# Optimization experiments

Hardware: AMD Instinct MI355X
Metric: run time of the kernel (lower is better)

The kernel has to match this reference:

```python
import jax, jax.numpy as jnp
import numpy as np

B, G, L, S = 4096, 16000, 64, 20000  # batch spots, genes, labels, total spots
LOG_2PI = float(np.log(2.0 * np.pi))


def _log_nb_positive_altparam(x, r, o):
    # NB with total_count r > 0 and logits o (stereoscope parametrization)
    return (jax.lax.lgamma(x + r) - jax.lax.lgamma(r) - jax.lax.lgamma(x + 1.0)
            + x * jax.nn.log_sigmoid(o) + r * jax.nn.log_sigmoid(-o))


def setup_inputs() -> dict:
    key = jax.random.key(0)
    ks = jax.random.split(key, 8)
    x = jax.random.randint(ks[0], (B, G), 0, 100, dtype=jnp.int32)
    y = jax.random.randint(ks[1], (B, 1), 0, L, dtype=jnp.int32)
    ind_x = jax.random.randint(ks[2], (B, 1), 0, S, dtype=jnp.int32)
    W = jax.random.normal(ks[3], (G, L), dtype=jnp.float32)          # fixed dictionary
    px_o = 0.5 * jax.random.normal(ks[4], (G,), dtype=jnp.float32)   # fixed log-odds
    eta = jax.random.normal(ks[5], (G,), dtype=jnp.float32)
    V = jax.random.normal(ks[6], (L + 1, S), dtype=jnp.float32)
    beta = 0.1 * jax.random.normal(ks[7], (G,), dtype=jnp.float32)
    return {"x": x, "y": y, "ind_x": ind_x, "W": W, "px_o": px_o,
            "eta": eta, "V": V, "beta": beta}


def reference(x, y, ind_x, W, px_o, eta, V, beta):
    x_f = x.astype(jnp.float32)                      # [B, G]
    beta_sp = jax.nn.softplus(beta)                  # [G]
    w_sp = jax.nn.softplus(W)                        # [G, L]
    eps_sp = jax.nn.softplus(eta)                    # [G]
    # r_hat = [beta*W | eps]  -> [G, L+1]
    r_hat = jnp.concatenate([beta_sp[:, None] * w_sp, eps_sp[:, None]], axis=1)
    # column-gather from V (embedding lookup over spots), then softplus
    v_ind = jax.nn.softplus(V[:, ind_x[:, 0]])       # [L+1, B]
    # thin matmul, inner dim L+1; px_rate: [B, G]
    px_rate = jnp.einsum("gl,lb->bg", r_hat, v_ind)
    # NB reconstruction loss per spot
    reconst_loss = -jnp.sum(_log_nb_positive_altparam(x_f, px_rate, px_o[None, :]), axis=-1)  # [B]
    # -sum log N(eta; 0, 1)
    neg_log_likelihood_prior = jnp.sum(0.5 * LOG_2PI + 0.5 * eta * eta)
    return (reconst_loss, jnp.float32(0.0), neg_log_likelihood_prior)
```

## Files before the change

### kernel.cpp

```cpp
#include <hip/hip_runtime.h>
#include <hip/hip_bf16.h>
#include <math.h>

#define Gn 16000
#define Bn 4096
#define Ln 64
#define Sn 20000

typedef __attribute__((ext_vector_type(8))) short bf16x8;
typedef __attribute__((ext_vector_type(4))) float f32x4;


__device__ __forceinline__ float softplus_precise(float z) {
    return fmaxf(z, 0.0f) + log1pf(__expf(-fabsf(z)));
}

__device__ __forceinline__ float lgamma_pos8(float z) {
    float p = z * (z + 1.f) * (z + 2.f) * (z + 3.f)
                * (z + 4.f) * (z + 5.f) * (z + 6.f) * (z + 7.f);
    float w = z + 8.f;
    return (w - 0.5f) * __logf(w) - w + 0.9189385332046727f
           + __fdividef(1.0f, 12.0f * w) - __logf(p);
}

__device__ __forceinline__ unsigned short f2bf(float f) {
    union { float f; unsigned int u; } v; v.f = f;
    unsigned int r = v.u + 0x7fff + ((v.u >> 16) & 1);
    return (unsigned short)(r >> 16);
}


__global__ void prep_genes(const float* __restrict__ W,
                           const float* __restrict__ px_o,
                           const float* __restrict__ eta,
                           const float* __restrict__ beta,
                           unsigned short* __restrict__ rhB,
                           float* __restrict__ lsp,
                           float* __restrict__ lsn,
                           float* __restrict__ eps) {
    int idx = blockIdx.x * 256 + threadIdx.x;
    int g = idx >> 6;
    float bsp = softplus_precise(beta[g]);
    rhB[idx] = f2bf(bsp * softplus_precise(W[idx]));
    if (idx < Gn) {
        eps[idx] = softplus_precise(eta[idx]);
        float o = px_o[idx];
        lsp[idx] = -softplus_precise(-o);
        lsn[idx] = -softplus_precise(o);
    }
}

__global__ void prep_spots(const float* __restrict__ V,
                           const int* __restrict__ ind_x,
                           unsigned short* __restrict__ vBg,
                           float* __restrict__ v64) {
    int idx = blockIdx.x * 256 + threadIdx.x;
    int b = idx >> 6, l = idx & 63;
    int s = ind_x[b];
    vBg[idx] = f2bf(softplus_precise(V[l * Sn + s]));
    if (idx < Bn) {
        int s2 = ind_x[idx];
        v64[idx] = softplus_precise(V[Ln * Sn + s2]);
    }
}

__global__ void prior_kernel(const float* __restrict__ eta, float* __restrict__ out) {
    int tid = threadIdx.x;
    float s = 0.f;
    for (int g = tid; g < Gn; g += 256) {
        float e = eta[g];
        s += 0.9189385332046727f + 0.5f * e * e;
    }
    #pragma unroll
    for (int off = 32; off; off >>= 1) s += __shfl_xor(s, off, 64);
    __shared__ float red[4];
    if ((tid & 63) == 0) red[tid >> 6] = s;
    __syncthreads();
    if (tid == 0) {
        out[Bn]     = 0.0f;
        out[Bn + 1] = red[0] + red[1] + red[2] + red[3];
    }
}


__global__ __launch_bounds__(256) void main_kernel(
    const int*            __restrict__ x,
    const unsigned short* __restrict__ rhB,
    const unsigned short* __restrict__ vBg,
    const float*          __restrict__ v64,
    const float*          __restrict__ lspg,
    const float*          __restrict__ lsng,
    const float*          __restrict__ epsg,
    float*                __restrict__ out) {
    __shared__ __align__(16) unsigned short sA[64][72];
    __shared__ __align__(16) unsigned short sB[64][72];
    __shared__ float sv64[64];
    __shared__ float sLsp[64], sLsn[64], sEps[64];
    __shared__ float lfact[100];

    const int tid = threadIdx.x;
    const int g0 = blockIdx.x * 64;
    const int b0 = blockIdx.y * 64;

    {
        int row = tid >> 3;
        int c   = (tid & 7) * 8;
        *(uint4*)&sA[row][c]      = *(const uint4*)&vBg[(b0 + row) * 64 + c];
        *(uint4*)&sA[row + 32][c] = *(const uint4*)&vBg[(b0 + row + 32) * 64 + c];
        *(uint4*)&sB[row][c]      = *(const uint4*)&rhB[(g0 + row) * 64 + c];
        *(uint4*)&sB[row + 32][c] = *(const uint4*)&rhB[(g0 + row + 32) * 64 + c];
    }
    if (tid < 64) {
        sv64[tid] = v64[b0 + tid];
        sLsp[tid] = lspg[g0 + tid];
        sLsn[tid] = lsng[g0 + tid];
        sEps[tid] = epsg[g0 + tid];
    }
    if (tid < 100) lfact[tid] = lgamma_pos8((float)tid + 1.0f);

    const int wave = tid >> 6, lane = tid & 63;
    const int quad = lane >> 4, ln = lane & 15;
    const int mrow  = wave * 16 + ln;
    const int brow0 = b0 + wave * 16 + quad * 4;

    int xv[4][4];
    #pragma unroll
    for (int nb = 0; nb < 4; nb++) {
        int g = g0 + nb * 16 + ln;
        #pragma unroll
        for (int r = 0; r < 4; r++)
            xv[nb][r] = x[(brow0 + r) * Gn + g];
    }

    f32x4 acc[4];
    #pragma unroll
    for (int nb = 0; nb < 4; nb++) acc[nb] = (f32x4){0.f, 0.f, 0.f, 0.f};

    __syncthreads();

    #pragma unroll
    for (int kb = 0; kb < 2; kb++) {
        bf16x8 af = *(const bf16x8*)&sA[mrow][kb * 32 + quad * 8];
        #pragma unroll
        for (int nb = 0; nb < 4; nb++) {
            bf16x8 bf = *(const bf16x8*)&sB[nb * 16 + ln][kb * 32 + quad * 8];
            acc[nb] = __builtin_amdgcn_mfma_f32_16x16x32_bf16(af, bf, acc[nb], 0, 0, 0);
        }
    }

    float vvr[4];
    #pragma unroll
    for (int r = 0; r < 4; r++) vvr[r] = sv64[wave * 16 + quad * 4 + r];

    float rowpart[4] = {0.f, 0.f, 0.f, 0.f};
    #pragma unroll
    for (int nb = 0; nb < 4; nb++) {
        const float lspv = sLsp[nb * 16 + ln];
        const float lsnv = sLsn[nb * 16 + ln];
        const float ev   = sEps[nb * 16 + ln];
        #pragma unroll
        for (int r = 0; r < 4; r++) {
            const float rr = fmaf(ev, vvr[r], acc[nb][r]);
            const int   xi = xv[nb][r];
            const float xf = (float)xi;
            const float s  = rr + xf;
            const float wr = rr + 4.f, wx = s + 4.f;
            const float Pr = rr * (rr + 1.f) * ((rr + 2.f) * (rr + 3.f));
            const float Px = s  * (s  + 1.f) * ((s  + 2.f) * (s  + 3.f));
            const float lnQ = __logf(__fdividef(Px, Pr));
            float D = fmaf(wx - 0.5f, __logf(wx), -fmaf(wr - 0.5f, __logf(wr), xf))
                      - lnQ - 0.0833333333f * __fdividef(xf, wx * wr);
            float term = D - lfact[xi] + fmaf(xf, lspv, rr * lsnv);
            rowpart[r] += term;
        }
    }

    #pragma unroll
    for (int r = 0; r < 4; r++) {
        float v = rowpart[r];
        v += __shfl_xor(v, 1, 64);
        v += __shfl_xor(v, 2, 64);
        v += __shfl_xor(v, 4, 64);
        v += __shfl_xor(v, 8, 64);
        if (ln == 0) atomicAdd(&out[brow0 + r], -v);
    }
}


extern "C" void kernel_launch(void* const* d_in, const int* in_sizes, int n_in,
                              void* d_out, int out_size, void* d_ws, size_t ws_size,
                              hipStream_t stream) {
    const int*   x     = (const int*)d_in[0];
    const int*   ind_x = (const int*)d_in[2];
    const float* W     = (const float*)d_in[3];
    const float* px_o  = (const float*)d_in[4];
    const float* eta   = (const float*)d_in[5];
    const float* V     = (const float*)d_in[6];
    const float* beta  = (const float*)d_in[7];
    float* out = (float*)d_out;

    char* wsb = (char*)d_ws;
    unsigned short* rhB = (unsigned short*)(wsb);
    unsigned short* vBg = (unsigned short*)(wsb + 2048000);
    float*          v64 = (float*)(wsb + 2572288);
    float*          lsp = (float*)(wsb + 2588672);
    float*          lsn = (float*)(wsb + 2652672);
    float*          eps = (float*)(wsb + 2716672);

    hipMemsetAsync(d_out, 0, Bn * sizeof(float), stream);

    prep_genes<<<(Gn * 64) / 256, 256, 0, stream>>>(W, px_o, eta, beta, rhB, lsp, lsn, eps);
    prep_spots<<<(Bn * 64) / 256, 256, 0, stream>>>(V, ind_x, vBg, v64);
    prior_kernel<<<1, 256, 0, stream>>>(eta, out);

    dim3 grid(Gn / 64, Bn / 64);
    main_kernel<<<grid, 256, 0, stream>>>(x, rhB, vBg, v64, lsp, lsn, eps, out);
}
```

Baseline: 480.1 us.

## Loop each block over eight spot tiles with double-buffered prefetch of x and V

Each main-kernel block now handles eight consecutive 64-spot tiles against a fixed 64-gene tile. The gene-side data (the rhB tile, log-sigmoid terms, eps, the lgamma table) is loaded once per block instead of once per tile. The next tile's x values and V fragments are prefetched into registers while the current tile is computed, with the A tile double-buffered in shared memory. The prior reduction is spread over many blocks with atomics. The cost is higher register pressure from holding prefetched x, a launch_bounds occupancy hint, and a grid eight times smaller in y, which could leave the GPU less fully used.

```diff
diff --git a/kernel.cpp b/kernel.cpp
--- a/kernel.cpp
+++ b/kernel.cpp
@@ -6,6 +6,8 @@
 #define Bn 4096
 #define Ln 64
 #define Sn 20000
+#define ITERS 8
+#define NYB (Bn / (64 * ITERS))
 
 typedef __attribute__((ext_vector_type(8))) short bf16x8;
 typedef __attribute__((ext_vector_type(4))) float f32x4;
@@ -65,25 +67,22 @@
 }
 
 __global__ void prior_kernel(const float* __restrict__ eta, float* __restrict__ out) {
-    int tid = threadIdx.x;
+    int idx = blockIdx.x * 256 + threadIdx.x;
     float s = 0.f;
-    for (int g = tid; g < Gn; g += 256) {
-        float e = eta[g];
-        s += 0.9189385332046727f + 0.5f * e * e;
+    if (idx < Gn) {
+        float e = eta[idx];
+        s = 0.9189385332046727f + 0.5f * e * e;
     }
     #pragma unroll
     for (int off = 32; off; off >>= 1) s += __shfl_xor(s, off, 64);
     __shared__ float red[4];
-    if ((tid & 63) == 0) red[tid >> 6] = s;
+    if ((threadIdx.x & 63) == 0) red[threadIdx.x >> 6] = s;
     __syncthreads();
-    if (tid == 0) {
-        out[Bn]     = 0.0f;
-        out[Bn + 1] = red[0] + red[1] + red[2] + red[3];
-    }
-}
-
-
-__global__ __launch_bounds__(256) void main_kernel(
+    if (threadIdx.x == 0) atomicAdd(&out[Bn + 1], red[0] + red[1] + red[2] + red[3]);
+}
+
+
+__global__ __launch_bounds__(256, 4) void main_kernel(
     const int*            __restrict__ x,
     const unsigned short* __restrict__ rhB,
     const unsigned short* __restrict__ vBg,
@@ -92,97 +91,127 @@
     const float*          __restrict__ lsng,
     const float*          __restrict__ epsg,
     float*                __restrict__ out) {
-    __shared__ __align__(16) unsigned short sA[64][72];
     __shared__ __align__(16) unsigned short sB[64][72];
-    __shared__ float sv64[64];
-    __shared__ float sLsp[64], sLsn[64], sEps[64];
+    __shared__ __align__(16) unsigned short sA[2][64][72];
+    __shared__ float sv64[2][64];
     __shared__ float lfact[100];
 
     const int tid = threadIdx.x;
     const int g0 = blockIdx.x * 64;
-    const int b0 = blockIdx.y * 64;
-
-    {
-        int row = tid >> 3;
-        int c   = (tid & 7) * 8;
-        *(uint4*)&sA[row][c]      = *(const uint4*)&vBg[(b0 + row) * 64 + c];
-        *(uint4*)&sA[row + 32][c] = *(const uint4*)&vBg[(b0 + row + 32) * 64 + c];
-        *(uint4*)&sB[row][c]      = *(const uint4*)&rhB[(g0 + row) * 64 + c];
-        *(uint4*)&sB[row + 32][c] = *(const uint4*)&rhB[(g0 + row + 32) * 64 + c];
-    }
-    if (tid < 64) {
-        sv64[tid] = v64[b0 + tid];
-        sLsp[tid] = lspg[g0 + tid];
-        sLsn[tid] = lsng[g0 + tid];
-        sEps[tid] = epsg[g0 + tid];
-    }
+    const int row = tid >> 3;
+    const int c   = (tid & 7) * 8;
+
+    *(uint4*)&sB[row][c]      = *(const uint4*)&rhB[(g0 + row) * 64 + c];
+    *(uint4*)&sB[row + 32][c] = *(const uint4*)&rhB[(g0 + row + 32) * 64 + c];
     if (tid < 100) lfact[tid] = lgamma_pos8((float)tid + 1.0f);
 
     const int wave = tid >> 6, lane = tid & 63;
     const int quad = lane >> 4, ln = lane & 15;
-    const int mrow  = wave * 16 + ln;
-    const int brow0 = b0 + wave * 16 + quad * 4;
-
+    const int mrow = wave * 16 + ln;
+    const int brow = wave * 16 + quad * 4;
+
+    float lspv[4], lsnv[4], ev4[4];
+    #pragma unroll
+    for (int nb = 0; nb < 4; nb++) {
+        int g = g0 + nb * 16 + ln;
+        lspv[nb] = lspg[g];
+        lsnv[nb] = lsng[g];
+        ev4[nb]  = epsg[g];
+    }
+
+    int b0 = blockIdx.y * (64 * ITERS);
+
+    uint4 va0 = *(const uint4*)&vBg[(b0 + row) * 64 + c];
+    uint4 va1 = *(const uint4*)&vBg[(b0 + row + 32) * 64 + c];
+    float sv = (tid < 64) ? v64[b0 + tid] : 0.f;
     int xv[4][4];
     #pragma unroll
     for (int nb = 0; nb < 4; nb++) {
         int g = g0 + nb * 16 + ln;
         #pragma unroll
         for (int r = 0; r < 4; r++)
-            xv[nb][r] = x[(brow0 + r) * Gn + g];
-    }
-
-    f32x4 acc[4];
-    #pragma unroll
-    for (int nb = 0; nb < 4; nb++) acc[nb] = (f32x4){0.f, 0.f, 0.f, 0.f};
-
-    __syncthreads();
-
-    #pragma unroll
-    for (int kb = 0; kb < 2; kb++) {
-        bf16x8 af = *(const bf16x8*)&sA[mrow][kb * 32 + quad * 8];
+            xv[nb][r] = x[(size_t)(b0 + brow + r) * Gn + g];
+    }
+
+    for (int it = 0; it < ITERS; ++it) {
+        const int buf = it & 1;
+        *(uint4*)&sA[buf][row][c]      = va0;
+        *(uint4*)&sA[buf][row + 32][c] = va1;
+        if (tid < 64) sv64[buf][tid] = sv;
+        __syncthreads();
+
+        const int bn0 = b0 + 64;
+        if (it + 1 < ITERS) {
+            va0 = *(const uint4*)&vBg[(bn0 + row) * 64 + c];
+            va1 = *(const uint4*)&vBg[(bn0 + row + 32) * 64 + c];
+            if (tid < 64) sv = v64[bn0 + tid];
+        }
+
+        f32x4 acc[4];
+        #pragma unroll
+        for (int nb = 0; nb < 4; nb++) acc[nb] = (f32x4){0.f, 0.f, 0.f, 0.f};
+        #pragma unroll
+        for (int kb = 0; kb < 2; kb++) {
+            bf16x8 af = *(const bf16x8*)&sA[buf][mrow][kb * 32 + quad * 8];
+            #pragma unroll
+            for (int nb = 0; nb < 4; nb++) {
+                bf16x8 bfr = *(const bf16x8*)&sB[nb * 16 + ln][kb * 32 + quad * 8];
+                acc[nb] = __builtin_amdgcn_mfma_f32_16x16x32_bf16(af, bfr, acc[nb], 0, 0, 0);
+            }
+        }
+
+        int xn[4][4];
+        if (it + 1 < ITERS) {
+            #pragma unroll
+            for (int nb = 0; nb < 4; nb++) {
+                int g = g0 + nb * 16 + ln;
+                #pragma unroll
+                for (int r = 0; r < 4; r++)
+                    xn[nb][r] = x[(size_t)(bn0 + brow + r) * Gn + g];
+            }
+        }
+
+        float vvr[4];
+        #pragma unroll
+        for (int r = 0; r < 4; r++) vvr[r] = sv64[buf][brow + r];
+
+        float rowpart[4] = {0.f, 0.f, 0.f, 0.f};
         #pragma unroll
         for (int nb = 0; nb < 4; nb++) {
-            bf16x8 bf = *(const bf16x8*)&sB[nb * 16 + ln][kb * 32 + quad * 8];
-            acc[nb] = __builtin_amdgcn_mfma_f32_16x16x32_bf16(af, bf, acc[nb], 0, 0, 0);
-        }
-    }
-
-    float vvr[4];
-    #pragma unroll
-    for (int r = 0; r < 4; r++) vvr[r] = sv64[wave * 16 + quad * 4 + r];
-
-    float rowpart[4] = {0.f, 0.f, 0.f, 0.f};
-    #pragma unroll
-    for (int nb = 0; nb < 4; nb++) {
-        const float lspv = sLsp[nb * 16 + ln];
-        const float lsnv = sLsn[nb * 16 + ln];
-        const float ev   = sEps[nb * 16 + ln];
+            #pragma unroll
+            for (int r = 0; r < 4; r++) {
+                const float rr = fmaf(ev4[nb], vvr[r], acc[nb][r]);
+                const int   xi = xv[nb][r];
+                const float xf = (float)xi;
+                const float s  = rr + xf;
+                const float wr = rr + 4.f, wx = s + 4.f;
+                const float Pr = rr * (rr + 1.f) * ((rr + 2.f) * (rr + 3.f));
+                const float Px = s  * (s  + 1.f) * ((s  + 2.f) * (s  + 3.f));
+                const float lnQ = __logf(__fdividef(Px, Pr));
+                float D = fmaf(wx - 0.5f, __logf(wx), -fmaf(wr - 0.5f, __logf(wr), xf))
+                          - lnQ - 0.0833333333f * __fdividef(xf, wx * wr);
+                float term = D - lfact[xi] + fmaf(xf, lspv[nb], rr * lsnv[nb]);
+                rowpart[r] += term;
+            }
+        }
+
         #pragma unroll
         for (int r = 0; r < 4; r++) {
-            const float rr = fmaf(ev, vvr[r], acc[nb][r]);
-            const int   xi = xv[nb][r];
-            const float xf = (float)xi;
-            const float s  = rr + xf;
-            const float wr = rr + 4.f, wx = s + 4.f;
-            const float Pr = rr * (rr + 1.f) * ((rr + 2.f) * (rr + 3.f));
-            const float Px = s  * (s  + 1.f) * ((s  + 2.f) * (s  + 3.f));
-            const float lnQ = __logf(__fdividef(Px, Pr));
-            float D = fmaf(wx - 0.5f, __logf(wx), -fmaf(wr - 0.5f, __logf(wr), xf))
-                      - lnQ - 0.0833333333f * __fdividef(xf, wx * wr);
-            float term = D - lfact[xi] + fmaf(xf, lspv, rr * lsnv);
-            rowpart[r] += term;
-        }
-    }
-
-    #pragma unroll
-    for (int r = 0; r < 4; r++) {
-        float v = rowpart[r];
-        v += __shfl_xor(v, 1, 64);
-        v += __shfl_xor(v, 2, 64);
-        v += __shfl_xor(v, 4, 64);
-        v += __shfl_xor(v, 8, 64);
-        if (ln == 0) atomicAdd(&out[brow0 + r], -v);
+            float v = rowpart[r];
+            v += __shfl_xor(v, 1, 64);
+            v += __shfl_xor(v, 2, 64);
+            v += __shfl_xor(v, 4, 64);
+            v += __shfl_xor(v, 8, 64);
+            if (ln == 0) atomicAdd(&out[b0 + brow + r], -v);
+        }
+
+        if (it + 1 < ITERS) {
+            #pragma unroll
+            for (int nb = 0; nb < 4; nb++)
+                #pragma unroll
+                for (int r = 0; r < 4; r++) xv[nb][r] = xn[nb][r];
+        }
+        b0 = bn0;
     }
 }
 
@@ -207,12 +236,12 @@
     float*          lsn = (float*)(wsb + 2652672);
     float*          eps = (float*)(wsb + 2716672);
 
-    hipMemsetAsync(d_out, 0, Bn * sizeof(float), stream);
+    hipMemsetAsync(d_out, 0, (Bn + 2) * sizeof(float), stream);
 
     prep_genes<<<(Gn * 64) / 256, 256, 0, stream>>>(W, px_o, eta, beta, rhB, lsp, lsn, eps);
     prep_spots<<<(Bn * 64) / 256, 256, 0, stream>>>(V, ind_x, vBg, v64);
-    prior_kernel<<<1, 256, 0, stream>>>(eta, out);
-
-    dim3 grid(Gn / 64, Bn / 64);
+    prior_kernel<<<(Gn + 255) / 256, 256, 0, stream>>>(eta, out);
+
+    dim3 grid(Gn / 64, NYB);
     main_kernel<<<grid, 256, 0, stream>>>(x, rhB, vBg, v64, lsp, lsn, eps, out);
 }
```

Result: no change. 481.3 us (+0.2%).
